# Optimization experiments

Measured on AMD Instinct MI355X. Metric: run time of the kernel, lower is better.

The kernel has to match this reference:

```python
import jax, jax.numpy as jnp
import numpy as np

B, N, D = 2048, 256, 2
HID = 256
MU, SIGMA = 0.1, 0.2  # concrete drift/diffusion for the abstract SDE: dX = mu*X dt + sigma*X dW


def _init_lin(key, fan_in, fan_out):
    return jax.random.normal(key, (fan_in, fan_out), dtype=jnp.float32) / np.sqrt(fan_in)


def setup_inputs() -> dict:
    key = jax.random.key(0)
    ks = jax.random.split(key, 8)
    ts = jnp.linspace(0.0, 1.0, N, dtype=jnp.float32)
    x0 = jax.random.normal(ks[0], (B, D), dtype=jnp.float32)
    eps = jax.random.normal(ks[1], (B, N, D), dtype=jnp.float32)  # raw unit gaussians
    return {
        "ts": ts, "x0": x0, "eps": eps,
        "fW0": _init_lin(ks[2], D + 1, HID), "fb0": jnp.zeros((HID,), jnp.float32),
        "fW1": _init_lin(ks[3], HID, HID), "fb1": jnp.zeros((HID,), jnp.float32),
        "fW2": _init_lin(ks[4], HID, 1), "fb2": jnp.zeros((1,), jnp.float32),
        "gW0": _init_lin(ks[5], D + 1, HID), "gb0": jnp.zeros((HID,), jnp.float32),
        "gW1": _init_lin(ks[6], HID, HID), "gb1": jnp.zeros((HID,), jnp.float32),
        "gW2": _init_lin(ks[7], HID, D), "gb2": jnp.zeros((D,), jnp.float32),
    }


def _mlp(tx, params):
    h = tx
    n = len(params)
    for i, (W, b) in enumerate(params):
        h = h @ W + b
        if i < n - 1:
            h = jax.nn.relu(h)
    return h


def _final(x):
    # concrete terminal condition g(X_T) = ||X_T||^2 (BaseFinal stand-in)
    return jnp.sum(x * x, axis=-1, keepdims=True)


def reference(ts, x0, eps, fW0, fb0, fW1, fb1, fW2, fb2, gW0, gb0, gW1, gb1, gW2, gb2):
    dt = ts[1:] - ts[:-1]                                  # (N-1,)
    dW = eps[:, : N - 1, :] * jnp.sqrt(dt)[None, :, None]  # (B, N-1, D) scaled increments

    def step(x, inp):
        dw_t, h = inp                                      # dw_t: (B,D), h: scalar
        x_new = x + MU * x * h + SIGMA * x * dw_t
        return x_new, x_new

    _, traj = jax.lax.scan(step, x0, (jnp.transpose(dW, (1, 0, 2)), dt))
    x = jnp.concatenate([x0[:, None, :], jnp.transpose(traj, (1, 0, 2))], axis=1)  # (B,N,D)
    # last increment slot is never filled in the torch loop -> zeros
    dW_full = jnp.concatenate([dW, jnp.zeros((B, 1, D), dW.dtype)], axis=1)        # (B,N,D)

    final_value = _final(x[:, -1, :])                      # (B,1)
    t = jnp.broadcast_to(ts[None, :, None], (B, N, 1))
    tx = jnp.concatenate([t, x], axis=2)                   # (B,N,D+1)

    Y = _mlp(tx, [(fW0, fb0), (fW1, fb1), (fW2, fb2)])     # (B,N,1)
    Z = _mlp(tx, [(gW0, gb0), (gW1, gb1), (gW2, gb2)])     # (B,N,D)

    # per-step targets: Y_{t+1} detached, final_value at the last step
    targets = jnp.concatenate(
        [jax.lax.stop_gradient(Y[:, 1:, :]), final_value[:, None, :]], axis=1)
    preds = Y + jnp.sum(Z * dW_full, axis=2, keepdims=True)  # (B,N,1)
    # sum over time of per-step MSE (mean over batch)
    loss = jnp.sum(jnp.mean((preds - targets) ** 2, axis=(0, 2)))
    return loss, Y, final_value
```

## Files before the change

kernel.cpp:

```cpp
#include <hip/hip_runtime.h>
#include <math.h>

#define B_ 2048
#define N_ 256
#define R_ (B_*N_)
#define MU_ 0.1f
#define SIGMA_ 0.2f
#define TILE_M 64
#define GRID_MLP 512
#define ITERS (R_ / TILE_M / GRID_MLP)

typedef __attribute__((ext_vector_type(4))) float f32x4;
typedef __attribute__((ext_vector_type(2))) int   i32x2;
typedef __attribute__((ext_vector_type(8))) int   i32x8;

__global__ void prep_weights(const float* __restrict__ fW1, const float* __restrict__ gW1,
                             unsigned int* __restrict__ wswz) {
    int idx = blockIdx.x * 256 + threadIdx.x;
    if (idx >= 2 * 16384) return;
    int m = idx >> 14, wi = idx & 16383;
    int frag = wi >> 9;
    int lane = (wi >> 3) & 63, q = wi & 7;
    int ki = frag >> 4, ct = frag & 15;
    int k = ki * 128 + (lane >> 4) * 32 + q * 4;
    int c = ct * 16 + (lane & 15);
    const float* W = m ? gW1 : fW1;
    float v0 = W[(k + 0) * 256 + c];
    float v1 = W[(k + 1) * 256 + c];
    float v2 = W[(k + 2) * 256 + c];
    float v3 = W[(k + 3) * 256 + c];
    int u = __builtin_amdgcn_cvt_pk_fp8_f32(v0, v1, 0, false);
    u = __builtin_amdgcn_cvt_pk_fp8_f32(v2, v3, u, true);
    wswz[idx] = (unsigned int)u;
}

__global__ void traj_kernel(const float* __restrict__ ts, const float* __restrict__ x0,
                            const float* __restrict__ eps, float* __restrict__ xs,
                            float* __restrict__ fv) {
    int gid = blockIdx.x * 256 + threadIdx.x;
    int b = gid >> 6, lane = gid & 63;
    int n0 = lane * 4;

    float t0 = ts[n0], t1 = ts[n0 + 1], t2 = ts[n0 + 2], t3 = ts[n0 + 3];
    float t4 = (n0 + 4 < N_) ? ts[n0 + 4] : t3;
    float h0 = t1 - t0, h1 = t2 - t1, h2 = t3 - t2, h3 = t4 - t3;
    float s0 = sqrtf(h0), s1 = sqrtf(h1), s2 = sqrtf(h2), s3 = sqrtf(h3);

    const float4* e4 = (const float4*)(eps + (size_t)(b * N_ + n0) * 2);
    float4 ea = e4[0], eb = e4[1];
    float f0a = 1.f + MU_ * h0 + SIGMA_ * (ea.x * s0);
    float f0b = 1.f + MU_ * h0 + SIGMA_ * (ea.y * s0);
    float f1a = 1.f + MU_ * h1 + SIGMA_ * (ea.z * s1);
    float f1b = 1.f + MU_ * h1 + SIGMA_ * (ea.w * s1);
    float f2a = 1.f + MU_ * h2 + SIGMA_ * (eb.x * s2);
    float f2b = 1.f + MU_ * h2 + SIGMA_ * (eb.y * s2);
    float f3a = 1.f + MU_ * h3 + SIGMA_ * (eb.z * s3);
    float f3b = 1.f + MU_ * h3 + SIGMA_ * (eb.w * s3);

    float Pa = f0a * f1a * f2a * f3a;
    float Pb = f0b * f1b * f2b * f3b;
    float Sa = Pa, Sb = Pb;
#pragma unroll
    for (int d = 1; d < 64; d <<= 1) {
        float va = __shfl_up(Sa, d);
        float vb = __shfl_up(Sb, d);
        if (lane >= d) { Sa *= va; Sb *= vb; }
    }
    float Ea = __shfl_up(Sa, 1);
    float Eb = __shfl_up(Sb, 1);
    if (lane == 0) { Ea = 1.f; Eb = 1.f; }

    float x0a = x0[2 * b], x0b = x0[2 * b + 1];
    float xa0 = x0a * Ea, xb0 = x0b * Eb;
    float xa1 = xa0 * f0a, xb1 = xb0 * f0b;
    float xa2 = xa1 * f1a, xb2 = xb1 * f1b;
    float xa3 = xa2 * f2a, xb3 = xb2 * f2b;

    float4* xsv = (float4*)(xs + (size_t)(b * N_ + n0) * 2);
    xsv[0] = make_float4(xa0, xb0, xa1, xb1);
    xsv[1] = make_float4(xa2, xb2, xa3, xb3);
    if (lane == 63) fv[b] = xa3 * xa3 + xb3 * xb3;
}

__global__ __launch_bounds__(512) void mlp_kernel(
        const float* __restrict__ ts, const float* __restrict__ eps, const float* __restrict__ xs,
        const unsigned int* __restrict__ wswz,
        const float* __restrict__ fW0, const float* __restrict__ fb0,
        const float* __restrict__ fb1, const float* __restrict__ fW2, const float* __restrict__ fb2,
        const float* __restrict__ gW0, const float* __restrict__ gb0,
        const float* __restrict__ gb1, const float* __restrict__ gW2, const float* __restrict__ gb2,
        float* __restrict__ Yout, float* __restrict__ zdot) {

    __shared__ __align__(16) unsigned char h0s[2][TILE_M * 256];
    __shared__ __align__(16) float4 sfx[TILE_M * ITERS];
    __shared__ __align__(16) float2 sd[TILE_M * ITERS];
    __shared__ __align__(16) float red2[2][TILE_M][36];

    const int MLP = blockIdx.x & 1;
    const int bid = blockIdx.x >> 1;

    const float* W0 = MLP ? gW0 : fW0;
    const float* b0 = MLP ? gb0 : fb0;
    const float* b1 = MLP ? gb1 : fb1;
    const float* W2 = MLP ? gW2 : fW2;
    const float* b2 = MLP ? gb2 : fb2;
    float* outp     = MLP ? zdot : Yout;

    const int tid  = threadIdx.x;
    const int lane = tid & 63;
    const int w    = tid >> 6;
    const int arow = lane & 15;
    const int rg   = lane >> 4;

    const int c0 = (tid & 63) * 4;
    const int row0 = (tid >> 6) * 8;
    f32x4 w0t = *(const f32x4*)(W0 + c0);
    f32x4 w0x = *(const f32x4*)(W0 + 256 + c0);
    f32x4 w0y = *(const f32x4*)(W0 + 512 + c0);
    f32x4 w0bv = *(const f32x4*)(b0 + c0);

    f32x4 bi0 = *(const f32x4*)(b1 + w * 32 + 4 * rg);
    f32x4 bi1 = *(const f32x4*)(b1 + w * 32 + 16 + 4 * rg);
    f32x4 w20v[2], w21v[2];
#pragma unroll
    for (int p = 0; p < 2; ++p) {
        int c = w * 32 + p * 16 + 4 * rg;
        if (MLP) {
            f32x4 lo = *(const f32x4*)(W2 + 2 * c);
            f32x4 hi = *(const f32x4*)(W2 + 2 * c + 4);
            w20v[p] = (f32x4){lo[0], lo[2], hi[0], hi[2]};
            w21v[p] = (f32x4){lo[1], lo[3], hi[1], hi[3]};
        } else {
            w20v[p] = *(const f32x4*)(W2 + c);
            w21v[p] = (f32x4){0.f, 0.f, 0.f, 0.f};
        }
    }
    const float b20 = b2[0];
    const float b21 = MLP ? b2[1] : 0.f;

    i32x8 afrag[2][2];
    {
        const i32x2* wsw2 = (const i32x2*)(wswz + MLP * 16384);
#pragma unroll
        for (int ki = 0; ki < 2; ++ki)
#pragma unroll
            for (int p = 0; p < 2; ++p) {
                int base = ((ki * 16 + (w * 2 + p)) * 64 + lane) * 4;
                i32x2 a0 = wsw2[base], a1 = wsw2[base + 1], a2 = wsw2[base + 2], a3 = wsw2[base + 3];
                afrag[ki][p] = (i32x8){a0[0], a0[1], a1[0], a1[1], a2[0], a2[1], a3[0], a3[1]};
            }
    }

#pragma unroll
    for (int q = 0; q < 2; ++q) {
        int s = q * 512 + tid;
        int it = s >> 6, i = s & 63;
        int r = (bid + it * GRID_MLP) * TILE_M + i;
        int n = r & (N_ - 1);
        float2 xv = ((const float2*)xs)[r];
        float tv = ts[n];
        sfx[s] = make_float4(tv, xv.x, xv.y, 0.f);
        if (MLP) {
            float sdt = (n < N_ - 1) ? sqrtf(ts[n + 1] - tv) : 0.f;
            float2 ev = ((const float2*)eps)[r];
            sd[s] = make_float2(ev.x * sdt, ev.y * sdt);
        }
    }
    __syncthreads();

#pragma unroll
    for (int ii = 0; ii < 8; ++ii) {
        int r = row0 + ii;
        float4 v = sfx[r];
        f32x4 h;
#pragma unroll
        for (int j = 0; j < 4; ++j)
            h[j] = fmaxf(fmaf(v.x, w0t[j], fmaf(v.y, w0x[j], fmaf(v.z, w0y[j], w0bv[j]))), 0.f);
        int q = __builtin_amdgcn_cvt_pk_fp8_f32(h[0], h[1], 0, false);
        q = __builtin_amdgcn_cvt_pk_fp8_f32(h[2], h[3], q, true);
        int off = r * 256 + (c0 ^ ((r & 15) << 3));
        *(unsigned int*)(h0s[0] + off) = (unsigned int)q;
    }
    __syncthreads();

    for (int t = 0; t < ITERS; ++t) {
        const int sb = t & 1;

        if (t > 0 && tid < TILE_M) {
            const int pb = sb ^ 1;
            const float* rr = red2[pb][tid];
            float s = 0.f;
#pragma unroll
            for (int j = 0; j < 32; j += 4) {
                f32x4 v = *(const f32x4*)(rr + j);
                s += (v[0] + v[1]) + (v[2] + v[3]);
            }
            if (!MLP) s += b20;
            outp[(bid + (t - 1) * GRID_MLP) * TILE_M + tid] = s;
        }

        f32x4 acc[4][2];
#pragma unroll
        for (int rt = 0; rt < 4; ++rt) { acc[rt][0] = bi0; acc[rt][1] = bi1; }
        __builtin_amdgcn_s_setprio(1);
#pragma unroll
        for (int ki = 0; ki < 2; ++ki) {
#pragma unroll
            for (int rt = 0; rt < 4; ++rt) {
                int row = rt * 16 + arow;
                const int rsw = (row & 15) << 3;
                const unsigned char* bp = h0s[sb] + row * 256;
                const int kb = ki * 128 + rg * 32;
                i32x2 q0 = *(const i32x2*)(bp + ((kb +  0) ^ rsw));
                i32x2 q1 = *(const i32x2*)(bp + ((kb +  8) ^ rsw));
                i32x2 q2 = *(const i32x2*)(bp + ((kb + 16) ^ rsw));
                i32x2 q3 = *(const i32x2*)(bp + ((kb + 24) ^ rsw));
                i32x8 bf = (i32x8){q0[0], q0[1], q1[0], q1[1], q2[0], q2[1], q3[0], q3[1]};
                acc[rt][0] = __builtin_amdgcn_mfma_scale_f32_16x16x128_f8f6f4(
                                 afrag[ki][0], bf, acc[rt][0], 0, 0, 0, 127, 0, 127);
                acc[rt][1] = __builtin_amdgcn_mfma_scale_f32_16x16x128_f8f6f4(
                                 afrag[ki][1], bf, acc[rt][1], 0, 0, 0, 127, 0, 127);
            }
        }
        __builtin_amdgcn_s_setprio(0);

#pragma unroll
        for (int rt = 0; rt < 4; ++rt) {
            float A0 = 0.f, A1 = 0.f;
#pragma unroll
            for (int p = 0; p < 2; ++p) {
#pragma unroll
                for (int i = 0; i < 4; ++i) {
                    float v = fmaxf(acc[rt][p][i], 0.f);
                    A0 = fmaf(v, w20v[p][i], A0);
                    if (MLP) A1 = fmaf(v, w21v[p][i], A1);
                }
            }
            int row = rt * 16 + arow;
            float rv;
            if (MLP) {
                float2 dv = sd[t * TILE_M + row];
                rv = fmaf(A1, dv.y, A0 * dv.x);
                if (w == 0) rv += fmaf(b21, dv.y, b20 * dv.x);
            } else {
                rv = A0;
            }
            red2[sb][row][w * 4 + rg] = rv;
        }

        if (t + 1 < ITERS) {
            const int sbase = (t + 1) * TILE_M;
#pragma unroll
            for (int ii = 0; ii < 8; ++ii) {
                int r = row0 + ii;
                float4 v = sfx[sbase + r];
                f32x4 h;
#pragma unroll
                for (int j = 0; j < 4; ++j)
                    h[j] = fmaxf(fmaf(v.x, w0t[j], fmaf(v.y, w0x[j], fmaf(v.z, w0y[j], w0bv[j]))), 0.f);
                int q = __builtin_amdgcn_cvt_pk_fp8_f32(h[0], h[1], 0, false);
                q = __builtin_amdgcn_cvt_pk_fp8_f32(h[2], h[3], q, true);
                int off = r * 256 + (c0 ^ ((r & 15) << 3));
                *(unsigned int*)(h0s[sb ^ 1] + off) = (unsigned int)q;
            }
        }
        __syncthreads();
    }
    if (tid < TILE_M) {
        const int pb = (ITERS - 1) & 1;
        const float* rr = red2[pb][tid];
        float s = 0.f;
#pragma unroll
        for (int j = 0; j < 32; j += 4) {
            f32x4 v = *(const f32x4*)(rr + j);
            s += (v[0] + v[1]) + (v[2] + v[3]);
        }
        if (!MLP) s += b20;
        outp[(bid + (ITERS - 1) * GRID_MLP) * TILE_M + tid] = s;
    }
}

__global__ void loss_partial_kernel(const float* __restrict__ Yout, const float* __restrict__ fv,
                                    const float* __restrict__ zdot, float* __restrict__ partials) {
    __shared__ float wred[4];
    int tid = threadIdx.x;
    float s = 0.f;
    for (int r = blockIdx.x * 256 + tid; r < R_; r += gridDim.x * 256) {
        int n = r & (N_ - 1);
        float pred = Yout[r] + zdot[r];
        float target = (n == N_ - 1) ? fv[r >> 8] : Yout[r + 1];
        float d = pred - target;
        s = fmaf(d, d, s);
    }
#pragma unroll
    for (int m = 1; m < 64; m <<= 1) s += __shfl_xor(s, m);
    if ((tid & 63) == 0) wred[tid >> 6] = s;
    __syncthreads();
    if (tid == 0) partials[blockIdx.x] = wred[0] + wred[1] + wred[2] + wred[3];
}

__global__ void loss_final_kernel(const float* __restrict__ partials, float* __restrict__ out) {
    __shared__ float wred[4];
    int tid = threadIdx.x;
    float s = partials[tid] + partials[256 + tid] + partials[512 + tid] + partials[768 + tid];
#pragma unroll
    for (int m = 1; m < 64; m <<= 1) s += __shfl_xor(s, m);
    if ((tid & 63) == 0) wred[tid >> 6] = s;
    __syncthreads();
    if (tid == 0) out[0] = (wred[0] + wred[1] + wred[2] + wred[3]) * (1.0f / B_);
}

extern "C" void kernel_launch(void* const* d_in, const int* in_sizes, int n_in,
                              void* d_out, int out_size, void* d_ws, size_t ws_size,
                              hipStream_t stream) {
    const float* ts  = (const float*)d_in[0];
    const float* x0  = (const float*)d_in[1];
    const float* eps = (const float*)d_in[2];
    const float* fW0 = (const float*)d_in[3];
    const float* fb0 = (const float*)d_in[4];
    const float* fW1 = (const float*)d_in[5];
    const float* fb1 = (const float*)d_in[6];
    const float* fW2 = (const float*)d_in[7];
    const float* fb2 = (const float*)d_in[8];
    const float* gW0 = (const float*)d_in[9];
    const float* gb0 = (const float*)d_in[10];
    const float* gW1 = (const float*)d_in[11];
    const float* gb1 = (const float*)d_in[12];
    const float* gW2 = (const float*)d_in[13];
    const float* gb2 = (const float*)d_in[14];

    float* out  = (float*)d_out;
    float* Yout = out + 1;
    float* fv   = out + 1 + R_;

    char* wsb = (char*)d_ws;
    float* xs           = (float*)wsb;
    unsigned int* wswz  = (unsigned int*)(wsb + (4 << 20));
    float* zdot         = (float*)(wsb + (4 << 20) + (256 << 10));
    float* partials     = (float*)(wsb + (4 << 20) + (256 << 10) + (2 << 20));

    hipLaunchKernelGGL(prep_weights, dim3(128), dim3(256), 0, stream, fW1, gW1, wswz);
    hipLaunchKernelGGL(traj_kernel, dim3(512), dim3(256), 0, stream, ts, x0, eps, xs, fv);
    hipLaunchKernelGGL(mlp_kernel, dim3(2 * GRID_MLP), dim3(512), 0, stream,
                       ts, eps, xs, wswz,
                       fW0, fb0, fb1, fW2, fb2,
                       gW0, gb0, gb1, gW2, gb2, Yout, zdot);
    hipLaunchKernelGGL(loss_partial_kernel, dim3(1024), dim3(256), 0, stream, Yout, fv, zdot, partials);
    hipLaunchKernelGGL(loss_final_kernel, dim3(1), dim3(256), 0, stream, partials, out);
}
```

Measured before the change: 154.4 us.

## Use 1024-thread MLP blocks with 2x8 wave grid and shuffle-based row reduction

Halves the MLP grid and doubles the block size to 16 waves. The waves are arranged as 2 row-halves by 8 column groups, so each wave handles 32 rows instead of 64 and the per-wave accumulator count is halved. The per-row partial sums are now reduced across the four lane groups with xor shuffles before the shared-memory write, which shrinks the reduction buffer from 32 to 8 partials per row. In exchange, each block carries twice as many waves and handles twice as many tiles per block, which changes occupancy, synchronisation cost and shared-memory use.

```diff
diff --git a/kernel.cpp b/kernel.cpp
--- a/kernel.cpp
+++ b/kernel.cpp
@@ -7,7 +7,7 @@
 #define MU_ 0.1f
 #define SIGMA_ 0.2f
 #define TILE_M 64
-#define GRID_MLP 512
+#define GRID_MLP 256
 #define ITERS (R_ / TILE_M / GRID_MLP)
 
 typedef __attribute__((ext_vector_type(4))) float f32x4;
@@ -82,7 +82,7 @@
     if (lane == 63) fv[b] = xa3 * xa3 + xb3 * xb3;
 }
 
-__global__ __launch_bounds__(512) void mlp_kernel(
+__global__ __launch_bounds__(1024) void mlp_kernel(
         const float* __restrict__ ts, const float* __restrict__ eps, const float* __restrict__ xs,
         const unsigned int* __restrict__ wswz,
         const float* __restrict__ fW0, const float* __restrict__ fb0,
@@ -94,7 +94,7 @@
     __shared__ __align__(16) unsigned char h0s[2][TILE_M * 256];
     __shared__ __align__(16) float4 sfx[TILE_M * ITERS];
     __shared__ __align__(16) float2 sd[TILE_M * ITERS];
-    __shared__ __align__(16) float red2[2][TILE_M][36];
+    __shared__ __align__(16) float red[2][TILE_M][12];
 
     const int MLP = blockIdx.x & 1;
     const int bid = blockIdx.x >> 1;
@@ -109,22 +109,24 @@
     const int tid  = threadIdx.x;
     const int lane = tid & 63;
     const int w    = tid >> 6;
+    const int wr   = w & 1;
+    const int wc   = w >> 1;
     const int arow = lane & 15;
     const int rg   = lane >> 4;
 
     const int c0 = (tid & 63) * 4;
-    const int row0 = (tid >> 6) * 8;
+    const int row0 = (tid >> 6) * 4;
     f32x4 w0t = *(const f32x4*)(W0 + c0);
     f32x4 w0x = *(const f32x4*)(W0 + 256 + c0);
     f32x4 w0y = *(const f32x4*)(W0 + 512 + c0);
     f32x4 w0bv = *(const f32x4*)(b0 + c0);
 
-    f32x4 bi0 = *(const f32x4*)(b1 + w * 32 + 4 * rg);
-    f32x4 bi1 = *(const f32x4*)(b1 + w * 32 + 16 + 4 * rg);
+    f32x4 bi0 = *(const f32x4*)(b1 + wc * 32 + 4 * rg);
+    f32x4 bi1 = *(const f32x4*)(b1 + wc * 32 + 16 + 4 * rg);
     f32x4 w20v[2], w21v[2];
 #pragma unroll
     for (int p = 0; p < 2; ++p) {
-        int c = w * 32 + p * 16 + 4 * rg;
+        int c = wc * 32 + p * 16 + 4 * rg;
         if (MLP) {
             f32x4 lo = *(const f32x4*)(W2 + 2 * c);
             f32x4 hi = *(const f32x4*)(W2 + 2 * c + 4);
@@ -145,7 +147,7 @@
         for (int ki = 0; ki < 2; ++ki)
 #pragma unroll
             for (int p = 0; p < 2; ++p) {
-                int base = ((ki * 16 + (w * 2 + p)) * 64 + lane) * 4;
+                int base = ((ki * 16 + (wc * 2 + p)) * 64 + lane) * 4;
                 i32x2 a0 = wsw2[base], a1 = wsw2[base + 1], a2 = wsw2[base + 2], a3 = wsw2[base + 3];
                 afrag[ki][p] = (i32x8){a0[0], a0[1], a1[0], a1[1], a2[0], a2[1], a3[0], a3[1]};
             }
@@ -153,7 +155,7 @@
 
 #pragma unroll
     for (int q = 0; q < 2; ++q) {
-        int s = q * 512 + tid;
+        int s = q * 1024 + tid;
         int it = s >> 6, i = s & 63;
         int r = (bid + it * GRID_MLP) * TILE_M + i;
         int n = r & (N_ - 1);
@@ -169,7 +171,7 @@
     __syncthreads();
 
 #pragma unroll
-    for (int ii = 0; ii < 8; ++ii) {
+    for (int ii = 0; ii < 4; ++ii) {
         int r = row0 + ii;
         float4 v = sfx[r];
         f32x4 h;
@@ -188,26 +190,23 @@
 
         if (t > 0 && tid < TILE_M) {
             const int pb = sb ^ 1;
-            const float* rr = red2[pb][tid];
-            float s = 0.f;
-#pragma unroll
-            for (int j = 0; j < 32; j += 4) {
-                f32x4 v = *(const f32x4*)(rr + j);
-                s += (v[0] + v[1]) + (v[2] + v[3]);
-            }
+            const float* rr = red[pb][tid];
+            f32x4 v0 = *(const f32x4*)(rr + 0);
+            f32x4 v1 = *(const f32x4*)(rr + 4);
+            float s = ((v0[0] + v0[1]) + (v0[2] + v0[3])) + ((v1[0] + v1[1]) + (v1[2] + v1[3]));
             if (!MLP) s += b20;
             outp[(bid + (t - 1) * GRID_MLP) * TILE_M + tid] = s;
         }
 
-        f32x4 acc[4][2];
-#pragma unroll
-        for (int rt = 0; rt < 4; ++rt) { acc[rt][0] = bi0; acc[rt][1] = bi1; }
+        f32x4 acc[2][2];
+#pragma unroll
+        for (int rt = 0; rt < 2; ++rt) { acc[rt][0] = bi0; acc[rt][1] = bi1; }
         __builtin_amdgcn_s_setprio(1);
 #pragma unroll
         for (int ki = 0; ki < 2; ++ki) {
 #pragma unroll
-            for (int rt = 0; rt < 4; ++rt) {
-                int row = rt * 16 + arow;
+            for (int rt = 0; rt < 2; ++rt) {
+                int row = wr * 32 + rt * 16 + arow;
                 const int rsw = (row & 15) << 3;
                 const unsigned char* bp = h0s[sb] + row * 256;
                 const int kb = ki * 128 + rg * 32;
@@ -225,7 +224,7 @@
         __builtin_amdgcn_s_setprio(0);
 
 #pragma unroll
-        for (int rt = 0; rt < 4; ++rt) {
+        for (int rt = 0; rt < 2; ++rt) {
             float A0 = 0.f, A1 = 0.f;
 #pragma unroll
             for (int p = 0; p < 2; ++p) {
@@ -236,22 +235,26 @@
                     if (MLP) A1 = fmaf(v, w21v[p][i], A1);
                 }
             }
-            int row = rt * 16 + arow;
-            float rv;
-            if (MLP) {
-                float2 dv = sd[t * TILE_M + row];
-                rv = fmaf(A1, dv.y, A0 * dv.x);
-                if (w == 0) rv += fmaf(b21, dv.y, b20 * dv.x);
-            } else {
-                rv = A0;
-            }
-            red2[sb][row][w * 4 + rg] = rv;
+            A0 += __shfl_xor(A0, 16); A0 += __shfl_xor(A0, 32);
+            if (MLP) { A1 += __shfl_xor(A1, 16); A1 += __shfl_xor(A1, 32); }
+            if (rg == 0) {
+                int row = wr * 32 + rt * 16 + arow;
+                float rv;
+                if (MLP) {
+                    float2 dv = sd[t * TILE_M + row];
+                    rv = fmaf(A1, dv.y, A0 * dv.x);
+                    if (wc == 0) rv += fmaf(b21, dv.y, b20 * dv.x);
+                } else {
+                    rv = A0;
+                }
+                red[sb][row][wc] = rv;
+            }
         }
 
         if (t + 1 < ITERS) {
             const int sbase = (t + 1) * TILE_M;
 #pragma unroll
-            for (int ii = 0; ii < 8; ++ii) {
+            for (int ii = 0; ii < 4; ++ii) {
                 int r = row0 + ii;
                 float4 v = sfx[sbase + r];
                 f32x4 h;
@@ -268,13 +271,10 @@
     }
     if (tid < TILE_M) {
         const int pb = (ITERS - 1) & 1;
-        const float* rr = red2[pb][tid];
-        float s = 0.f;
-#pragma unroll
-        for (int j = 0; j < 32; j += 4) {
-            f32x4 v = *(const f32x4*)(rr + j);
-            s += (v[0] + v[1]) + (v[2] + v[3]);
-        }
+        const float* rr = red[pb][tid];
+        f32x4 v0 = *(const f32x4*)(rr + 0);
+        f32x4 v1 = *(const f32x4*)(rr + 4);
+        float s = ((v0[0] + v0[1]) + (v0[2] + v0[3])) + ((v1[0] + v1[1]) + (v1[2] + v1[3]));
         if (!MLP) s += b20;
         outp[(bid + (ITERS - 1) * GRID_MLP) * TILE_M + tid] = s;
     }
@@ -341,7 +341,7 @@
 
     hipLaunchKernelGGL(prep_weights, dim3(128), dim3(256), 0, stream, fW1, gW1, wswz);
     hipLaunchKernelGGL(traj_kernel, dim3(512), dim3(256), 0, stream, ts, x0, eps, xs, fv);
-    hipLaunchKernelGGL(mlp_kernel, dim3(2 * GRID_MLP), dim3(512), 0, stream,
+    hipLaunchKernelGGL(mlp_kernel, dim3(2 * GRID_MLP), dim3(1024), 0, stream,
                        ts, eps, xs, wswz,
                        fW0, fb0, fb1, fW2, fb2,
                        gW0, gb0, gb1, gW2, gb2, Yout, zdot);
```

Measured after the change: 344.3 us. 2.23x slower.
